# Performance work log

Measured on AMD Instinct MI355X. Metric: run time of the kernel, lower is better.

The kernel has to match this reference:

```python
import jax, jax.numpy as jnp
import numpy as np

COST_CLASS = 1.0
COST_L1 = 1.0


def _lsa(cost):
    """Exact rectangular linear sum assignment (Jonker-Volgenant / e-maxx Hungarian).
    cost: (n, m) numpy float64 with n <= m. Returns ans[n]: column assigned to each row.
    """
    n, m = cost.shape
    INF = np.inf
    u = np.zeros(n + 1)
    v = np.zeros(m + 1)
    p = np.zeros(m + 1, dtype=np.int64)    # p[j]: 1-indexed row matched to column j (0 = free)
    way = np.zeros(m + 1, dtype=np.int64)
    for i in range(1, n + 1):
        p[0] = i
        j0 = 0
        minv = np.full(m + 1, INF)
        used = np.zeros(m + 1, dtype=bool)
        while True:
            used[j0] = True
            i0 = p[j0]
            minv1 = minv[1:]               # view, in-place updates propagate
            jmask = ~used[1:]
            cur = cost[i0 - 1, :] - u[i0] - v[1:]
            upd = jmask & (cur < minv1)
            minv1[upd] = cur[upd]
            way[1:][upd] = j0
            idx = np.nonzero(jmask)[0]
            j1rel = idx[np.argmin(minv1[idx])]
            delta = minv1[j1rel]
            u[p[used]] += delta
            v[used] -= delta
            minv1[jmask] -= delta
            j0 = j1rel + 1
            if p[j0] == 0:
                break
        # augment along the alternating path
        while j0:
            j1 = way[j0]
            p[j0] = p[j1]
            j0 = j1
    ans = np.zeros(n, dtype=np.int64)
    for j in range(1, m + 1):
        if p[j] > 0:
            ans[p[j] - 1] = j - 1
    return ans


def _solve_blocks(blocks):
    """blocks: (B, Q, T) numpy. Per-batch optimal assignment, scipy-compatible output:
    row_ind sorted ascending, min(Q,T) pairs (here Q >= T so T pairs)."""
    blocks = np.asarray(blocks, dtype=np.float64)
    B, Q, T = blocks.shape
    rows = np.empty((B, T), dtype=np.int32)
    cols = np.empty((B, T), dtype=np.int32)
    for b in range(B):
        c = blocks[b]
        if Q >= T:
            ans = _lsa(c.T)                      # ans[t] = matched query q
            order = np.argsort(ans, kind="stable")
            rows[b] = ans[order]
            cols[b] = order
        else:
            ans = _lsa(c)
            rows[b] = np.arange(Q)
            cols[b] = ans
    return rows, cols


def _cost_blocks(outputs, targets):
    """Diagonal (per-sample) blocks of the DETR cost matrix.
    outputs: (B, Q, 1+P); targets: (B, T, 1+P). Returns (B, Q, T).
    Math identical to building the full (B*Q, B*T) matrix and slicing, as in the source."""
    out_prob = jax.nn.softmax(outputs[:, :, 0], axis=-1)      # softmax over the QUERY axis (as in source)
    out_pos = outputs[:, :, 1:]                                # (B, Q, P)
    tgt_pos = targets[:, :, 1:]                                # (B, T, P)
    cost_l1 = jnp.abs(out_pos[:, :, None, :] - tgt_pos[:, None, :, :]).sum(-1)  # L1 cdist, (B, Q, T)
    return COST_CLASS * (-out_prob[:, :, None]) + COST_L1 * cost_l1


def setup_inputs() -> dict:
    key = jax.random.key(0)
    k1, k2 = jax.random.split(key)
    outputs = jax.random.normal(k1, (8, 2048, 3), dtype=jnp.float32)
    targets = jax.random.uniform(k2, (8, 256, 3), dtype=jnp.float32)
    return {"outputs": outputs, "targets": targets}


def reference(outputs, targets):
    blocks = _cost_blocks(outputs, targets)                    # (B, Q, T)
    B, Q, T = blocks.shape
    n = min(Q, T)
    shapes = (jax.ShapeDtypeStruct((B, n), jnp.int32),
              jax.ShapeDtypeStruct((B, n), jnp.int32))
    row_ind, col_ind = jax.pure_callback(_solve_blocks, shapes, blocks)
    return row_ind, col_ind
```

## Files before the change

kernel.cpp:

```cpp
#include <hip/hip_runtime.h>


constexpr int B = 8;
constexpr int Q = 2048;
constexpr int T = 256;
constexpr int NT = 256;
constexpr int KPT = Q / NT;
constexpr int NW = NT / 64;

struct __align__(16) CD { double u; float tx, ty; };

__device__ __forceinline__ unsigned wave_min_u32_dpp(unsigned a) {
  int v = (int)a, t;
  t = __builtin_amdgcn_update_dpp(v, v, 0x111, 0xf, 0xf, false);
  v = ((unsigned)t < (unsigned)v) ? t : v;
  t = __builtin_amdgcn_update_dpp(v, v, 0x112, 0xf, 0xf, false);
  v = ((unsigned)t < (unsigned)v) ? t : v;
  t = __builtin_amdgcn_update_dpp(v, v, 0x114, 0xf, 0xf, false);
  v = ((unsigned)t < (unsigned)v) ? t : v;
  t = __builtin_amdgcn_update_dpp(v, v, 0x118, 0xf, 0xf, false);
  v = ((unsigned)t < (unsigned)v) ? t : v;
  t = __builtin_amdgcn_update_dpp(v, v, 0x142, 0xf, 0xf, false);
  v = ((unsigned)t < (unsigned)v) ? t : v;
  t = __builtin_amdgcn_update_dpp(v, v, 0x143, 0xf, 0xf, false);
  v = ((unsigned)t < (unsigned)v) ? t : v;
  return (unsigned)__builtin_amdgcn_readlane(v, 63);
}

__launch_bounds__(NT, 1)
__global__ void hungarian_r12(const float* __restrict__ outs,
                              const float* __restrict__ tgts,
                              int* __restrict__ out) {
  const int b = blockIdx.x;
  const int tid = threadIdx.x;
  const int lane = tid & 63;
  const int wv = tid >> 6;

  __shared__ CD colDat[Q + 1];
  __shared__ float2 rowTgt[T + 1];
  __shared__ short p[Q + 1];
  __shared__ uint4 pk[2][NW];
  __shared__ double vdelta[Q];
  __shared__ int ansArr[T];
  __shared__ double s_rv[NW];
  __shared__ float sh_f;

  const size_t qbase = (size_t)b * Q;
  const size_t tbase = (size_t)b * T;

  float xs[KPT], qx[KPT], qy[KPT];
#pragma unroll
  for (int k = 0; k < KPT; ++k) {
    const size_t o = (qbase + tid + k * NT) * 3;
    xs[k] = outs[o];
    qx[k] = outs[o + 1];
    qy[k] = outs[o + 2];
  }
  {
    const size_t o = (tbase + tid) * 3;
    rowTgt[tid + 1] = make_float2(tgts[o + 1], tgts[o + 2]);
    if (tid == 0) rowTgt[0] = make_float2(0.f, 0.f);
  }

  float lmax = xs[0];
#pragma unroll
  for (int k = 1; k < KPT; ++k) lmax = fmaxf(lmax, xs[k]);
  for (int off = 32; off > 0; off >>= 1) lmax = fmaxf(lmax, __shfl_down(lmax, off));
  if ((tid & 63) == 0) s_rv[tid >> 6] = (double)lmax;
  __syncthreads();
  if (tid == 0) {
    float m2 = (float)s_rv[0];
    for (int w = 1; w < NW; ++w) m2 = fmaxf(m2, (float)s_rv[w]);
    sh_f = m2;
  }
  __syncthreads();
  const float smax = sh_f;
  float ex[KPT];
  float lsum = 0.f;
#pragma unroll
  for (int k = 0; k < KPT; ++k) { ex[k] = expf(xs[k] - smax); lsum += ex[k]; }
  for (int off = 32; off > 0; off >>= 1) lsum += __shfl_down(lsum, off);
  if ((tid & 63) == 0) s_rv[tid >> 6] = (double)lsum;
  __syncthreads();
  if (tid == 0) {
    float s2 = 0.f;
    for (int w = 0; w < NW; ++w) s2 += (float)s_rv[w];
    sh_f = s2;
  }
  __syncthreads();
  const float ssum = sh_f;
  float np_[KPT];
#pragma unroll
  for (int k = 0; k < KPT; ++k) np_[k] = -(ex[k] / ssum);

  for (int j = tid; j <= Q; j += NT) {
    p[j] = 0;
    CD c0; c0.u = 0.0; c0.tx = -1.0f; c0.ty = 0.0f;
    colDat[j] = c0;
  }
  double vreg[KPT];
#pragma unroll
  for (int k = 0; k < KPT; ++k) {
    vreg[k] = 0.0;
    vdelta[tid + (k << 8)] = 0.0;
  }
  __syncthreads();

  const float FINF = __int_as_float(0x7f800000);
  float2 nxtT = rowTgt[1];

  for (int i = 1; i <= T; ++i) {
    unsigned usedMask = 0;
    double D = 0.0;
    int i0 = i;
    double ui0 = 0.0;
    float tX = nxtT.x, tY = nxtT.y;
    int s = 0, S;
    int j1v = 0;
    int recRow = 0, recCol = 0, recPrev = 0;
    double recU = 0.0, recD = 0.0;
    float recTX = 0.f, recTY = 0.f;

    for (;;) {
      if (tid == s) {
        recRow = i0; recU = ui0; recTX = tX; recTY = tY; recD = D; recPrev = j1v;
      }

      double cv[KPT];
#pragma unroll
      for (int k = 0; k < KPT; ++k) {
        float cf = fabsf(qx[k] - tX) + fabsf(qy[k] - tY) + np_[k];
        if (usedMask & (1u << k)) cf = FINF;
        cv[k] = ((double)cf - ui0) - vreg[k];
      }
      const double m01 = fmin(cv[0], cv[1]), m23 = fmin(cv[2], cv[3]);
      const double m45 = fmin(cv[4], cv[5]), m67 = fmin(cv[6], cv[7]);
      const double m03 = fmin(m01, m23), m47 = fmin(m45, m67);
      double bval = fmin(m03, m47);
      unsigned emsk = 0;
#pragma unroll
      for (int k = 0; k < KPT; ++k) emsk |= (cv[k] == bval) ? (1u << k) : 0u;
      const int bk = (int)__builtin_ctz(emsk);
      int bidx = 1 + tid + (bk << 8);

      bval += 0.0;
      const long long bb = __double_as_longlong(bval);
      const unsigned long long key = (unsigned long long)bb ^
          ((bb < 0) ? 0xFFFFFFFFFFFFFFFFull : 0x8000000000000000ull);
      const unsigned khi = (unsigned)(key >> 32);
      const unsigned klo = (unsigned)key;

      const unsigned minhi = wave_min_u32_dpp(khi);
      const unsigned long long mask = __ballot(khi == minhi);
      int wl;
      if (__popcll(mask) == 1) {
        wl = (int)__ffsll(mask) - 1;
      } else {
        unsigned wklo = 0xffffffffu; int widx = 0x7fffffff; wl = 0;
        unsigned long long mm = mask;
        while (mm) {
          const int l = (int)__ffsll(mm) - 1; mm &= mm - 1;
          const unsigned lo2 = (unsigned)__builtin_amdgcn_readlane((int)klo, l);
          const int ix2 = __builtin_amdgcn_readlane(bidx, l);
          if (lo2 < wklo || (lo2 == wklo && ix2 < widx)) {
            wklo = lo2; widx = ix2; wl = l;
          }
        }
      }
      const int par = s & 1;
      if (lane == wl) pk[par][wv] = make_uint4(minhi, klo, (unsigned)bidx, 0u);
      __syncthreads();

      const uint4 c0v = pk[par][0];
      const uint4 c1v = pk[par][1];
      const uint4 c2v = pk[par][2];
      const uint4 c3v = pk[par][3];
      const CD cd0 = colDat[(int)c0v.z];
      const CD cd1 = colDat[(int)c1v.z];
      const CD cd2 = colDat[(int)c2v.z];
      const CD cd3 = colDat[(int)c3v.z];

      const unsigned long long k0b = ((unsigned long long)c0v.x << 32) | c0v.y;
      const unsigned long long k1b = ((unsigned long long)c1v.x << 32) | c1v.y;
      const unsigned long long k2b = ((unsigned long long)c2v.x << 32) | c2v.y;
      const unsigned long long k3b = ((unsigned long long)c3v.x << 32) | c3v.y;
      const int j0b = (int)c0v.z, j1bb = (int)c1v.z;
      const int j2b = (int)c2v.z, j3b = (int)c3v.z;
      const bool w01 = (k1b < k0b) || (k1b == k0b && j1bb < j0b);
      const unsigned long long k01 = w01 ? k1b : k0b;
      const int j01 = w01 ? j1bb : j0b;
      const bool w23 = (k3b < k2b) || (k3b == k2b && j3b < j2b);
      const unsigned long long k23 = w23 ? k3b : k2b;
      const int j23 = w23 ? j3b : j2b;
      const bool wf = (k23 < k01) || (k23 == k01 && j23 < j01);
      const unsigned long long bkk = wf ? k23 : k01;
      const int j1 = wf ? j23 : j01;
      CD cdA; cdA.u = w01 ? cd1.u : cd0.u;
      cdA.tx = w01 ? cd1.tx : cd0.tx; cdA.ty = w01 ? cd1.ty : cd0.ty;
      CD cdB; cdB.u = w23 ? cd3.u : cd2.u;
      cdB.tx = w23 ? cd3.tx : cd2.tx; cdB.ty = w23 ? cd3.ty : cd2.ty;
      CD cd; cd.u = wf ? cdB.u : cdA.u;
      cd.tx = wf ? cdB.tx : cdA.tx; cd.ty = wf ? cdB.ty : cdA.ty;

      const long long db = (long long)((bkk & 0x8000000000000000ull)
                                           ? (bkk ^ 0x8000000000000000ull) : ~bkk);
      D += __longlong_as_double(db);
      if (tid == ((j1 - 1) & 255)) usedMask |= 1u << ((j1 - 1) >> 8);
      if (tid == s) recCol = j1;
      const int pj1 = (int)p[j1];
      j1v = j1;
      ++s;
      if (cd.tx < 0.0f) { S = s; break; }
      ui0 = cd.u; tX = cd.tx; tY = cd.ty; i0 = pj1;
    }

    __syncthreads();
    nxtT = rowTgt[i < T ? i + 1 : T];
    const double Dfin = D;
    if (tid < S) {
      p[recCol] = (short)recRow;
      const double unew = recU + (Dfin - recD);
      CD c2; c2.u = unew; c2.tx = recTX; c2.ty = recTY;
      colDat[recCol] = c2;
      if (tid >= 1) {
        vdelta[recPrev - 1] = Dfin - recD;
      }
    }
    __syncthreads();
#pragma unroll
    for (int k = 0; k < KPT; ++k) {
      const double dv = vdelta[tid + (k << 8)];
      vreg[k] -= dv;
      vdelta[tid + (k << 8)] = 0.0;
    }
  }
  __syncthreads();

  for (int j = 1 + tid; j <= Q; j += NT) {
    const int pi = (int)p[j];
    if (pi > 0) ansArr[pi - 1] = j - 1;
  }
  __syncthreads();
  const int a = ansArr[tid];
  int rank = 0;
  for (int t2 = 0; t2 < T; ++t2) rank += (ansArr[t2] < a) ? 1 : 0;
  out[(size_t)b * T + rank] = a;
  out[(size_t)B * T + (size_t)b * T + rank] = tid;
}

extern "C" void kernel_launch(void* const* d_in, const int* in_sizes, int n_in,
                              void* d_out, int out_size, void* d_ws, size_t ws_size,
                              hipStream_t stream) {
  const float* outs = (const float*)d_in[0];
  const float* tgts = (const float*)d_in[1];
  int* out = (int*)d_out;
  hungarian_r12<<<B, NT, 0, stream>>>(outs, tgts, out);
}
```

Baseline: 866.7 us.

## Keep per-column row data in registers and skip barriers on trivial augments

Moves each column's matched-row data (u, target x/y) out of a shared colDat array and into per-thread registers. The owning lane now picks it during the local argmin and publishes it in the per-wave candidate slot, so the dependent shared-memory load after the barrier in the inner Dijkstra step goes away. When the augmenting path has length one, the update is done only by the owning thread and both end-of-row barriers are skipped. Longer paths still go through shared staging slots that every thread then merges into its registers. The cost is more register pressure and larger per-wave candidate writes.

```diff
diff --git a/kernel.cpp b/kernel.cpp
--- a/kernel.cpp
+++ b/kernel.cpp
@@ -8,8 +8,6 @@
 constexpr int KPT = Q / NT;
 constexpr int NW = NT / 64;
 
-struct __align__(16) CD { double u; float tx, ty; };
-
 __device__ __forceinline__ unsigned wave_min_u32_dpp(unsigned a) {
   int v = (int)a, t;
   t = __builtin_amdgcn_update_dpp(v, v, 0x111, 0xf, 0xf, false);
@@ -28,7 +26,7 @@
 }
 
 __launch_bounds__(NT, 1)
-__global__ void hungarian_r12(const float* __restrict__ outs,
+__global__ void hungarian_r13(const float* __restrict__ outs,
                               const float* __restrict__ tgts,
                               int* __restrict__ out) {
   const int b = blockIdx.x;
@@ -36,11 +34,13 @@
   const int lane = tid & 63;
   const int wv = tid >> 6;
 
-  __shared__ CD colDat[Q + 1];
   __shared__ float2 rowTgt[T + 1];
   __shared__ short p[Q + 1];
-  __shared__ uint4 pk[2][NW];
+  __shared__ uint4 pk2[2][NW][2];
   __shared__ double vdelta[Q];
+  __shared__ double slotU[Q];
+  __shared__ float slotX[Q];
+  __shared__ float slotY[Q];
   __shared__ int ansArr[T];
   __shared__ double s_rv[NW];
   __shared__ float sh_f;
@@ -93,21 +93,23 @@
 #pragma unroll
   for (int k = 0; k < KPT; ++k) np_[k] = -(ex[k] / ssum);
 
-  for (int j = tid; j <= Q; j += NT) {
-    p[j] = 0;
-    CD c0; c0.u = 0.0; c0.tx = -1.0f; c0.ty = 0.0f;
-    colDat[j] = c0;
-  }
+  for (int j = tid; j <= Q; j += NT) p[j] = 0;
   double vreg[KPT];
+  double cdu[KPT];
+  float cdx[KPT], cdy[KPT];
 #pragma unroll
   for (int k = 0; k < KPT; ++k) {
     vreg[k] = 0.0;
-    vdelta[tid + (k << 8)] = 0.0;
+    cdu[k] = 0.0; cdx[k] = -1.0f; cdy[k] = 0.0f;
+    const int a = tid + (k << 8);
+    vdelta[a] = 0.0;
+    slotU[a] = 0.0; slotX[a] = -2.0f; slotY[a] = 0.0f;
   }
   __syncthreads();
 
   const float FINF = __int_as_float(0x7f800000);
   float2 nxtT = rowTgt[1];
+  int par = 0;
 
   for (int i = 1; i <= T; ++i) {
     unsigned usedMask = 0;
@@ -122,6 +124,8 @@
     float recTX = 0.f, recTY = 0.f;
 
     for (;;) {
+      const int cpar = par; par ^= 1;
+
       if (tid == s) {
         recRow = i0; recU = ui0; recTX = tX; recTY = tY; recD = D; recPrev = j1v;
       }
@@ -142,6 +146,20 @@
       for (int k = 0; k < KPT; ++k) emsk |= (cv[k] == bval) ? (1u << k) : 0u;
       const int bk = (int)__builtin_ctz(emsk);
       int bidx = 1 + tid + (bk << 8);
+
+      const int b0 = bk & 1, b1 = (bk >> 1) & 1, b2 = (bk >> 2) & 1;
+      const double uA = b0 ? cdu[1] : cdu[0], uB = b0 ? cdu[3] : cdu[2];
+      const double uC = b0 ? cdu[5] : cdu[4], uD = b0 ? cdu[7] : cdu[6];
+      const float xA = b0 ? cdx[1] : cdx[0], xB = b0 ? cdx[3] : cdx[2];
+      const float xC = b0 ? cdx[5] : cdx[4], xD = b0 ? cdx[7] : cdx[6];
+      const float yA = b0 ? cdy[1] : cdy[0], yB = b0 ? cdy[3] : cdy[2];
+      const float yC = b0 ? cdy[5] : cdy[4], yD = b0 ? cdy[7] : cdy[6];
+      const double uE = b1 ? uB : uA, uF = b1 ? uD : uC;
+      const float xE = b1 ? xB : xA, xF = b1 ? xD : xC;
+      const float yE = b1 ? yB : yA, yF = b1 ? yD : yC;
+      const double csu = b2 ? uF : uE;
+      const float csx = b2 ? xF : xE;
+      const float csy = b2 ? yF : yE;
 
       bval += 0.0;
       const long long bb = __double_as_longlong(bval);
@@ -167,18 +185,24 @@
           }
         }
       }
-      const int par = s & 1;
-      if (lane == wl) pk[par][wv] = make_uint4(minhi, klo, (unsigned)bidx, 0u);
+      if (lane == wl) {
+        pk2[cpar][wv][0] = make_uint4(minhi, klo, (unsigned)bidx, 0u);
+        const unsigned long long cu =
+            (unsigned long long)__double_as_longlong(csu);
+        pk2[cpar][wv][1] = make_uint4((unsigned)cu, (unsigned)(cu >> 32),
+                                      __float_as_uint(csx),
+                                      __float_as_uint(csy));
+      }
       __syncthreads();
 
-      const uint4 c0v = pk[par][0];
-      const uint4 c1v = pk[par][1];
-      const uint4 c2v = pk[par][2];
-      const uint4 c3v = pk[par][3];
-      const CD cd0 = colDat[(int)c0v.z];
-      const CD cd1 = colDat[(int)c1v.z];
-      const CD cd2 = colDat[(int)c2v.z];
-      const CD cd3 = colDat[(int)c3v.z];
+      const uint4 c0v = pk2[cpar][0][0];
+      const uint4 c1v = pk2[cpar][1][0];
+      const uint4 c2v = pk2[cpar][2][0];
+      const uint4 c3v = pk2[cpar][3][0];
+      const uint4 d0v = pk2[cpar][0][1];
+      const uint4 d1v = pk2[cpar][1][1];
+      const uint4 d2v = pk2[cpar][2][1];
+      const uint4 d3v = pk2[cpar][3][1];
 
       const unsigned long long k0b = ((unsigned long long)c0v.x << 32) | c0v.y;
       const unsigned long long k1b = ((unsigned long long)c1v.x << 32) | c1v.y;
@@ -195,12 +219,16 @@
       const bool wf = (k23 < k01) || (k23 == k01 && j23 < j01);
       const unsigned long long bkk = wf ? k23 : k01;
       const int j1 = wf ? j23 : j01;
-      CD cdA; cdA.u = w01 ? cd1.u : cd0.u;
-      cdA.tx = w01 ? cd1.tx : cd0.tx; cdA.ty = w01 ? cd1.ty : cd0.ty;
-      CD cdB; cdB.u = w23 ? cd3.u : cd2.u;
-      cdB.tx = w23 ? cd3.tx : cd2.tx; cdB.ty = w23 ? cd3.ty : cd2.ty;
-      CD cd; cd.u = wf ? cdB.u : cdA.u;
-      cd.tx = wf ? cdB.tx : cdA.tx; cd.ty = wf ? cdB.ty : cdA.ty;
+      const unsigned ulA = w01 ? d1v.x : d0v.x, uhA = w01 ? d1v.y : d0v.y;
+      const unsigned xAf = w01 ? d1v.z : d0v.z, yAf = w01 ? d1v.w : d0v.w;
+      const unsigned ulB = w23 ? d3v.x : d2v.x, uhB = w23 ? d3v.y : d2v.y;
+      const unsigned xBf = w23 ? d3v.z : d2v.z, yBf = w23 ? d3v.w : d2v.w;
+      const unsigned ulW = wf ? ulB : ulA, uhW = wf ? uhB : uhA;
+      const unsigned xW = wf ? xBf : xAf, yW = wf ? yBf : yAf;
+      const double cdun = __longlong_as_double(
+          (long long)(((unsigned long long)uhW << 32) | ulW));
+      const float cdtx = __uint_as_float(xW);
+      const float cdty = __uint_as_float(yW);
 
       const long long db = (long long)((bkk & 0x8000000000000000ull)
                                            ? (bkk ^ 0x8000000000000000ull) : ~bkk);
@@ -210,28 +238,50 @@
       const int pj1 = (int)p[j1];
       j1v = j1;
       ++s;
-      if (cd.tx < 0.0f) { S = s; break; }
-      ui0 = cd.u; tX = cd.tx; tY = cd.ty; i0 = pj1;
+      if (cdtx < 0.0f) { S = s; break; }
+      ui0 = cdun; tX = cdtx; tY = cdty; i0 = pj1;
     }
 
-    __syncthreads();
     nxtT = rowTgt[i < T ? i + 1 : T];
-    const double Dfin = D;
-    if (tid < S) {
-      p[recCol] = (short)recRow;
-      const double unew = recU + (Dfin - recD);
-      CD c2; c2.u = unew; c2.tx = recTX; c2.ty = recTY;
-      colDat[recCol] = c2;
-      if (tid >= 1) {
-        vdelta[recPrev - 1] = Dfin - recD;
-      }
-    }
-    __syncthreads();
-#pragma unroll
-    for (int k = 0; k < KPT; ++k) {
-      const double dv = vdelta[tid + (k << 8)];
-      vreg[k] -= dv;
-      vdelta[tid + (k << 8)] = 0.0;
+    if (S == 1) {
+      const int c = j1v - 1;
+      if (tid == (c & 255)) {
+        p[j1v] = (short)i;
+        const int ok = c >> 8;
+#pragma unroll
+        for (int k = 0; k < KPT; ++k) {
+          if (k == ok) { cdu[k] = D; cdx[k] = tX; cdy[k] = tY; }
+        }
+      }
+    } else {
+      const double Dfin = D;
+      if (tid < S) {
+        p[recCol] = (short)recRow;
+        const double unew = recU + (Dfin - recD);
+        const int c = recCol - 1;
+        slotU[c] = unew;
+        slotX[c] = recTX;
+        slotY[c] = recTY;
+        if (tid >= 1) {
+          vdelta[recPrev - 1] = Dfin - recD;
+        }
+      }
+      __syncthreads();
+#pragma unroll
+      for (int k = 0; k < KPT; ++k) {
+        const int a = tid + (k << 8);
+        const double dv = vdelta[a];
+        const float sx = slotX[a];
+        const double su = slotU[a];
+        const float sy = slotY[a];
+        vreg[k] -= dv;
+        vdelta[a] = 0.0;
+        slotX[a] = -2.0f;
+        const bool upd = (sx > -1.5f);
+        cdu[k] = upd ? su : cdu[k];
+        cdx[k] = upd ? sx : cdx[k];
+        cdy[k] = upd ? sy : cdy[k];
+      }
     }
   }
   __syncthreads();
@@ -254,5 +304,5 @@
   const float* outs = (const float*)d_in[0];
   const float* tgts = (const float*)d_in[1];
   int* out = (int*)d_out;
-  hungarian_r12<<<B, NT, 0, stream>>>(outs, tgts, out);
+  hungarian_r13<<<B, NT, 0, stream>>>(outs, tgts, out);
 }
```

Measured after the change: 1.134 ms. 1.31x slower.
